# Kernel tuning notes

Hardware: AMD Instinct MI355X
Metric: run time of the kernel (lower is better)

Reference implementation:

```python
import jax, jax.numpy as jnp
import numpy as np

N_EXPERTS = 8
D_IN = 2048
D_OUT = 2048
BATCH = 8192


def setup_inputs() -> dict:
    key = jax.random.key(0)
    k_x, k_w, k_b, k_a, k_m = jax.random.split(key, 5)
    xs = jax.random.normal(k_x, (BATCH, D_IN), dtype=jnp.float32)
    # Expert parameters: each submodule modeled as Linear(D_IN, D_OUT)
    W = jax.random.normal(k_w, (N_EXPERTS, D_IN, D_OUT), dtype=jnp.float32) / np.sqrt(D_IN)
    b = jax.random.normal(k_b, (N_EXPERTS, D_OUT), dtype=jnp.float32) * 0.01
    actions = jax.random.randint(k_a, (BATCH,), 0, N_EXPERTS, dtype=jnp.int32)
    mxs = jax.random.randint(k_m, (BATCH,), 0, N_EXPERTS, dtype=jnp.int32)  # pass-through metadata
    return {"xs": xs, "W": W, "b": b, "mxs": mxs, "actions": actions}


def reference(xs, W, b, mxs, actions):
    # Original: per-sample split, route sample i to submodule actions[i], concat.
    # Vectorized MoE dispatch-combine: compute all expert outputs, select by one-hot.
    onehot = jax.nn.one_hot(actions, W.shape[0], dtype=xs.dtype)  # [B, E]
    # y_all[b,e,f] = xs[b,:] @ W[e,:,:]; combine with one-hot selection, add routed bias.
    ys = jnp.einsum('be,bd,edf->bf', onehot, xs, W) + b[actions]  # [B, D_OUT]
    return (ys, mxs, actions)
```

## Files before the change

### kernel.cpp

```cpp
#include <hip/hip_runtime.h>
#include <hip/hip_bf16.h>
#include <stdint.h>

#define BATCH 8192
#define GROWS 9216
#define DIN   2048
#define DOUT  2048
#define NEXP  8
#define BM    128
#define BN    256
#define BK    32
#define NT    (DIN / BK)
#define NSLOT 72
#define BUFSZ 24576
#define BOFF  8192

typedef __attribute__((ext_vector_type(4))) float fx4;
typedef __attribute__((ext_vector_type(8))) short sx8;

__device__ __forceinline__ short f2b(float x){
  unsigned u = __float_as_uint(x);
  u = u + 0x7FFFu + ((u >> 16) & 1u);
  return (short)(u >> 16);
}

__device__ __forceinline__ void gload16(const void* g, void* l){
  __builtin_amdgcn_global_load_lds(
      (const __attribute__((address_space(1))) unsigned int*)g,
      (__attribute__((address_space(3))) unsigned int*)l, 16, 0, 0);
}

__global__ void prep_kernel(const int* __restrict__ actions, const int* __restrict__ mxs,
                            int* __restrict__ perm, int* __restrict__ meta,
                            float* __restrict__ out){
  __shared__ int cnt[NEXP], cur[NEXP];
  int t = threadIdx.x;
  for (int i = t; i < GROWS; i += 256) perm[i] = -1;
  if (t < NEXP) cnt[t] = 0;
  __syncthreads();
  for (int i = t; i < BATCH; i += 256){
    atomicAdd(&cnt[actions[i]], 1);
    out[(size_t)BATCH * DOUT + i]         = (float)mxs[i];
    out[(size_t)BATCH * DOUT + BATCH + i] = (float)actions[i];
  }
  __syncthreads();
  if (t == 0){
    int s = 0, slot = 0;
    for (int e = 0; e < NEXP; ++e){
      cur[e] = s;
      int ns = (cnt[e] + BM - 1) / BM;
      for (int q = 0; q < ns; ++q) meta[17 + slot++] = e;
      s += ns * BM;
    }
    meta[16] = slot;
  }
  __syncthreads();
  for (int i = t; i < BATCH; i += 256){
    int e = actions[i];
    perm[atomicAdd(&cur[e], 1)] = i;
  }
}

__global__ void gatherx_kernel(const float* __restrict__ xs, const int* __restrict__ perm,
                               short* __restrict__ xp){
  int i = blockIdx.x;
  int t = threadIdx.x;
  short v[8];
  int p = perm[i];
  if (p >= 0){
    const fx4* src = (const fx4*)(xs + (size_t)p * DIN + t * 8);
    fx4 a = src[0], b2 = src[1];
    v[0]=f2b(a.x); v[1]=f2b(a.y); v[2]=f2b(a.z); v[3]=f2b(a.w);
    v[4]=f2b(b2.x); v[5]=f2b(b2.y); v[6]=f2b(b2.z); v[7]=f2b(b2.w);
  } else {
#pragma unroll
    for (int j = 0; j < 8; ++j) v[j] = 0;
  }
  *(sx8*)(xp + (size_t)i * DIN + t * 8) = *(const sx8*)v;
}

__global__ void transw_kernel(const float* __restrict__ W, short* __restrict__ Wt){
  __shared__ float tile[64][69];
  int e  = blockIdx.z;
  int n0 = blockIdx.x * 64;
  int k0 = blockIdx.y * 64;
  const float* Wp = W + (size_t)e * DIN * DOUT + (size_t)k0 * DOUT + n0;
  int t = threadIdx.x;
#pragma unroll
  for (int it = 0; it < 4; ++it){
    int r = it * 16 + (t >> 4);
    int c = (t & 15) * 4;
    fx4 v = *(const fx4*)(Wp + (size_t)r * DOUT + c);
    tile[r][c] = v.x; tile[r][c+1] = v.y; tile[r][c+2] = v.z; tile[r][c+3] = v.w;
  }
  __syncthreads();
  int n  = t >> 2;
  int kc = (t & 3) * 16;
  short vv[16];
#pragma unroll
  for (int j = 0; j < 16; ++j) vv[j] = f2b(tile[kc + j][n]);
  short* dst = Wt + (size_t)e * DOUT * DIN + (size_t)(n0 + n) * DIN + k0 + kc;
  *(sx8*)dst       = *(const sx8*)vv;
  *(sx8*)(dst + 8) = *(const sx8*)(vv + 8);
}

__global__ __launch_bounds__(512, 4)
void moe_gemm_kernel(const short* __restrict__ xp, const short* __restrict__ Wt,
                     const float* __restrict__ bias, const int* __restrict__ perm,
                     const int* __restrict__ meta, float* __restrict__ out){
  __shared__ char lds[3 * BUFSZ];

  int F = blockIdx.x;
  int slot = F >> 3, nb = F & 7;
  int nslots = meta[16];
  if (slot >= nslots) return;
  int e      = meta[17 + slot];
  int m_base = slot * BM;
  int n0     = nb * BN;

  int t    = threadIdx.x;
  int wid  = t >> 6;
  int l    = t & 63;
  int wm   = wid & 1;
  int wn   = wid >> 1;
  int lrow = l & 15;
  int lk   = l >> 4;

  int srow = ((t >> 3) << 1) | ((t >> 2) & 1);
  int schk = (t & 3) ^ ((t >> 3) & 3);
  const char* ag  = (const char*)xp + ((size_t)(m_base + srow) * DIN + schk * 8) * 2;
  const char* bg0 = (const char*)Wt + (((size_t)e * DOUT + n0 + srow) * DIN + schk * 8) * 2;
  const char* bg1 = bg0 + (size_t)128 * DIN * 2;
  int ldst = t * 16;

#define STAGE(kt, BASE) do{ \
    gload16(ag  + (size_t)(kt) * 64, lds + (BASE) + ldst); \
    gload16(bg0 + (size_t)(kt) * 64, lds + (BASE) + BOFF + ldst); \
    gload16(bg1 + (size_t)(kt) * 64, lds + (BASE) + BOFF + 8192 + ldst); \
  }while(0)

  int arow = wm * 64 + lrow;
  int aline = arow >> 1;
  int addrA = aline * 128 + (arow & 1) * 64 + ((lk ^ (aline & 3)) << 4);
  int brow = wn * 64 + lrow;
  int bline = brow >> 1;
  int addrB = BOFF + bline * 128 + (brow & 1) * 64 + ((lk ^ (bline & 3)) << 4);

  fx4 acc[4][4];
#pragma unroll
  for (int m = 0; m < 4; ++m)
#pragma unroll
    for (int n = 0; n < 4; ++n)
      acc[m][n] = (fx4){0.f, 0.f, 0.f, 0.f};

  float bcol[4];
#pragma unroll
  for (int n = 0; n < 4; ++n)
    bcol[n] = bias[(size_t)e * DOUT + n0 + wn * 64 + n * 16 + lrow];

#define KSTEP(CB, SB, DOSTG, kt) do{ \
    sx8 af[4], bf[4]; \
    _Pragma("unroll") for (int m = 0; m < 4; ++m) \
      af[m] = *(const sx8*)(lds + (CB) + addrA + m * 1024); \
    _Pragma("unroll") for (int n = 0; n < 4; ++n) \
      bf[n] = *(const sx8*)(lds + (CB) + addrB + n * 1024); \
    if (DOSTG) STAGE((kt) + 2, SB); \
    __builtin_amdgcn_s_setprio(1); \
    _Pragma("unroll") for (int m = 0; m < 4; ++m) \
    _Pragma("unroll") for (int n = 0; n < 4; ++n) \
      acc[m][n] = __builtin_amdgcn_mfma_f32_16x16x32_bf16(af[m], bf[n], acc[m][n], 0, 0, 0); \
    __builtin_amdgcn_s_setprio(0); \
    if (DOSTG) asm volatile("s_waitcnt vmcnt(3)" ::: "memory"); \
    else       asm volatile("s_waitcnt vmcnt(0)" ::: "memory"); \
    __builtin_amdgcn_s_barrier(); \
    asm volatile("" ::: "memory"); \
  }while(0)

  STAGE(0, 0);
  STAGE(1, BUFSZ);
  asm volatile("s_waitcnt vmcnt(3)" ::: "memory");
  __builtin_amdgcn_s_barrier();
  asm volatile("" ::: "memory");

  for (int kt = 0; kt < 60; kt += 3){
    KSTEP(0,         2*BUFSZ, 1, kt);
    KSTEP(BUFSZ,     0,       1, kt + 1);
    KSTEP(2*BUFSZ,   BUFSZ,   1, kt + 2);
  }
  KSTEP(0,       2*BUFSZ, 1, 60);
  KSTEP(BUFSZ,   0,       1, 61);
  KSTEP(2*BUFSZ, 0,       0, 62);
  KSTEP(0,       0,       0, 63);

#pragma unroll
  for (int m = 0; m < 4; ++m){
    int rb = wm * 64 + m * 16 + lk * 4;
    int prow[4];
#pragma unroll
    for (int q = 0; q < 4; ++q)
      prow[q] = perm[m_base + rb + q];
#pragma unroll
    for (int n = 0; n < 4; ++n){
      int col = n0 + wn * 64 + n * 16 + lrow;
      fx4 v = acc[m][n];
#pragma unroll
      for (int q = 0; q < 4; ++q)
        if (prow[q] >= 0)
          out[(size_t)prow[q] * DOUT + col] = v[q] + bcol[n];
    }
  }
#undef KSTEP
#undef STAGE
}

extern "C" void kernel_launch(void* const* d_in, const int* in_sizes, int n_in,
                              void* d_out, int out_size, void* d_ws, size_t ws_size,
                              hipStream_t stream) {
  const float* xs      = (const float*)d_in[0];
  const float* W       = (const float*)d_in[1];
  const float* b       = (const float*)d_in[2];
  const int*   mxs     = (const int*)d_in[3];
  const int*   actions = (const int*)d_in[4];
  float* out = (float*)d_out;

  int*   perm = (int*)d_ws;
  int*   meta = (int*)((char*)d_ws + 40960);
  short* Wt   = (short*)((char*)d_ws + 65536);
  short* xp   = (short*)((char*)d_ws + 65536 + (size_t)NEXP * DIN * DOUT * 2);

  hipLaunchKernelGGL(prep_kernel, dim3(1), dim3(256), 0, stream, actions, mxs, perm, meta, out);
  hipLaunchKernelGGL(gatherx_kernel, dim3(GROWS), dim3(256), 0, stream, xs, perm, xp);
  hipLaunchKernelGGL(transw_kernel, dim3(DOUT/64, DIN/64, NEXP), dim3(256), 0, stream, W, Wt);
  hipLaunchKernelGGL(moe_gemm_kernel, dim3(NSLOT * 8), dim3(512), 0, stream,
                     xp, Wt, b, perm, meta, out);
}
```

Baseline: 190.5 us.

## Split prep into count and parallel scatter; deepen A prefetch with k-major LDS layout

The single-block prep kernel becomes a 1024-thread count kernel plus a 32-block scatter kernel that uses global atomics on per-expert cursors and also writes the pass-through outputs. The GEMM replaces the swizzled row-major LDS tiles with a k-chunk-major layout, uses separate ring buffers for A (4 deep) and B (3 deep), and prefetches A three tiles ahead. This is meant to cut serial prep time and hide global-load latency better. The costs are an extra kernel launch, a larger LDS footprint (80 KB) that may reduce occupancy, possible LDS bank conflicts from dropping the XOR swizzle, and a nondeterministic row order from the global atomics.

```diff
diff --git a/kernel.cpp b/kernel.cpp
--- a/kernel.cpp
+++ b/kernel.cpp
@@ -12,8 +12,13 @@
 #define BK    32
 #define NT    (DIN / BK)
 #define NSLOT 72
-#define BUFSZ 24576
-#define BOFF  8192
+#define AB0 0
+#define AB1 8192
+#define AB2 16384
+#define AB3 24576
+#define BB0 32768
+#define BB1 49152
+#define BB2 65536
 
 typedef __attribute__((ext_vector_type(4))) float fx4;
 typedef __attribute__((ext_vector_type(8))) short sx8;
@@ -30,34 +35,37 @@
       (__attribute__((address_space(3))) unsigned int*)l, 16, 0, 0);
 }
 
-__global__ void prep_kernel(const int* __restrict__ actions, const int* __restrict__ mxs,
-                            int* __restrict__ perm, int* __restrict__ meta,
-                            float* __restrict__ out){
-  __shared__ int cnt[NEXP], cur[NEXP];
+__global__ void prep_count(const int* __restrict__ actions, int* __restrict__ perm,
+                           int* __restrict__ meta){
+  __shared__ int cnt[NEXP];
   int t = threadIdx.x;
-  for (int i = t; i < GROWS; i += 256) perm[i] = -1;
   if (t < NEXP) cnt[t] = 0;
+  for (int i = t; i < GROWS; i += 1024) perm[i] = -1;
   __syncthreads();
-  for (int i = t; i < BATCH; i += 256){
-    atomicAdd(&cnt[actions[i]], 1);
-    out[(size_t)BATCH * DOUT + i]         = (float)mxs[i];
-    out[(size_t)BATCH * DOUT + BATCH + i] = (float)actions[i];
-  }
+  for (int i = t; i < BATCH; i += 1024) atomicAdd(&cnt[actions[i]], 1);
   __syncthreads();
   if (t == 0){
     int s = 0, slot = 0;
     for (int e = 0; e < NEXP; ++e){
-      cur[e] = s;
+      meta[e] = s;
       int ns = (cnt[e] + BM - 1) / BM;
       for (int q = 0; q < ns; ++q) meta[17 + slot++] = e;
       s += ns * BM;
     }
     meta[16] = slot;
   }
-  __syncthreads();
-  for (int i = t; i < BATCH; i += 256){
+}
+
+__global__ void prep_scatter(const int* __restrict__ actions, const int* __restrict__ mxs,
+                             int* __restrict__ perm, int* __restrict__ meta,
+                             float* __restrict__ out){
+  int i = blockIdx.x * 256 + threadIdx.x;
+  if (i < BATCH){
     int e = actions[i];
-    perm[atomicAdd(&cur[e], 1)] = i;
+    int p = atomicAdd(&meta[e], 1);
+    perm[p] = i;
+    out[(size_t)BATCH * DOUT + i]         = (float)mxs[i];
+    out[(size_t)BATCH * DOUT + BATCH + i] = (float)actions[i];
   }
 }
 
@@ -108,12 +116,11 @@
 void moe_gemm_kernel(const short* __restrict__ xp, const short* __restrict__ Wt,
                      const float* __restrict__ bias, const int* __restrict__ perm,
                      const int* __restrict__ meta, float* __restrict__ out){
-  __shared__ char lds[3 * BUFSZ];
+  __shared__ char lds[81920];
 
   int F = blockIdx.x;
   int slot = F >> 3, nb = F & 7;
-  int nslots = meta[16];
-  if (slot >= nslots) return;
+  if (slot >= meta[16]) return;
   int e      = meta[17 + slot];
   int m_base = slot * BM;
   int n0     = nb * BN;
@@ -126,25 +133,11 @@
   int lrow = l & 15;
   int lk   = l >> 4;
 
-  int srow = ((t >> 3) << 1) | ((t >> 2) & 1);
-  int schk = (t & 3) ^ ((t >> 3) & 3);
-  const char* ag  = (const char*)xp + ((size_t)(m_base + srow) * DIN + schk * 8) * 2;
-  const char* bg0 = (const char*)Wt + (((size_t)e * DOUT + n0 + srow) * DIN + schk * 8) * 2;
-  const char* bg1 = bg0 + (size_t)128 * DIN * 2;
-  int ldst = t * 16;
-
-#define STAGE(kt, BASE) do{ \
-    gload16(ag  + (size_t)(kt) * 64, lds + (BASE) + ldst); \
-    gload16(bg0 + (size_t)(kt) * 64, lds + (BASE) + BOFF + ldst); \
-    gload16(bg1 + (size_t)(kt) * 64, lds + (BASE) + BOFF + 8192 + ldst); \
-  }while(0)
-
-  int arow = wm * 64 + lrow;
-  int aline = arow >> 1;
-  int addrA = aline * 128 + (arow & 1) * 64 + ((lk ^ (aline & 3)) << 4);
-  int brow = wn * 64 + lrow;
-  int bline = brow >> 1;
-  int addrB = BOFF + bline * 128 + (brow & 1) * 64 + ((lk ^ (bline & 3)) << 4);
+  const char* ag = (const char*)xp + ((size_t)(m_base + (t & 127)) * DIN + (t >> 7) * 8) * 2;
+  const char* bg = (const char*)Wt + (((size_t)e * DOUT + n0 + (t & 255)) * DIN + (t >> 8) * 8) * 2;
+
+  int addrA = lk * 2048 + (wm * 64 + lrow) * 16;
+  int addrB = lk * 4096 + (wn * 64 + lrow) * 16;
 
   fx4 acc[4][4];
 #pragma unroll
@@ -158,39 +151,64 @@
   for (int n = 0; n < 4; ++n)
     bcol[n] = bias[(size_t)e * DOUT + n0 + wn * 64 + n * 16 + lrow];
 
-#define KSTEP(CB, SB, DOSTG, kt) do{ \
+#define STGA(KT, SA) gload16(ag + (size_t)(KT) * 64, lds + (SA) + (t << 4))
+#define STGB(KT, SB) do{ gload16(bg + (size_t)(KT) * 64,      lds + (SB) + (t << 4)); \
+                         gload16(bg + (size_t)(KT) * 64 + 32, lds + (SB) + 8192 + (t << 4)); }while(0)
+
+#define KSTEP(CA, CB, SA, SB, KT, DOB, DOA, VM) do{ \
+    if (DOB) STGB((KT) + 2, SB); \
+    if (DOA) STGA((KT) + 3, SA); \
     sx8 af[4], bf[4]; \
     _Pragma("unroll") for (int m = 0; m < 4; ++m) \
-      af[m] = *(const sx8*)(lds + (CB) + addrA + m * 1024); \
+      af[m] = *(const sx8*)(lds + (CA) + addrA + m * 256); \
     _Pragma("unroll") for (int n = 0; n < 4; ++n) \
-      bf[n] = *(const sx8*)(lds + (CB) + addrB + n * 1024); \
-    if (DOSTG) STAGE((kt) + 2, SB); \
+      bf[n] = *(const sx8*)(lds + (CB) + addrB + n * 256); \
     __builtin_amdgcn_s_setprio(1); \
     _Pragma("unroll") for (int m = 0; m < 4; ++m) \
     _Pragma("unroll") for (int n = 0; n < 4; ++n) \
       acc[m][n] = __builtin_amdgcn_mfma_f32_16x16x32_bf16(af[m], bf[n], acc[m][n], 0, 0, 0); \
     __builtin_amdgcn_s_setprio(0); \
-    if (DOSTG) asm volatile("s_waitcnt vmcnt(3)" ::: "memory"); \
-    else       asm volatile("s_waitcnt vmcnt(0)" ::: "memory"); \
+    asm volatile("s_waitcnt vmcnt(" #VM ")" ::: "memory"); \
     __builtin_amdgcn_s_barrier(); \
     asm volatile("" ::: "memory"); \
   }while(0)
 
-  STAGE(0, 0);
-  STAGE(1, BUFSZ);
-  asm volatile("s_waitcnt vmcnt(3)" ::: "memory");
+  STGA(0, AB0); STGB(0, BB0);
+  STGA(1, AB1); STGB(1, BB1);
+  STGA(2, AB2);
+  asm volatile("s_waitcnt vmcnt(4)" ::: "memory");
   __builtin_amdgcn_s_barrier();
   asm volatile("" ::: "memory");
 
-  for (int kt = 0; kt < 60; kt += 3){
-    KSTEP(0,         2*BUFSZ, 1, kt);
-    KSTEP(BUFSZ,     0,       1, kt + 1);
-    KSTEP(2*BUFSZ,   BUFSZ,   1, kt + 2);
-  }
-  KSTEP(0,       2*BUFSZ, 1, 60);
-  KSTEP(BUFSZ,   0,       1, 61);
-  KSTEP(2*BUFSZ, 0,       0, 62);
-  KSTEP(0,       0,       0, 63);
+  for (int kt = 0; kt < 60; kt += 12){
+    KSTEP(AB0, BB0, AB3, BB2, kt + 0,  1, 1, 4);
+    KSTEP(AB1, BB1, AB0, BB0, kt + 1,  1, 1, 4);
+    KSTEP(AB2, BB2, AB1, BB1, kt + 2,  1, 1, 4);
+    KSTEP(AB3, BB0, AB2, BB2, kt + 3,  1, 1, 4);
+    KSTEP(AB0, BB1, AB3, BB0, kt + 4,  1, 1, 4);
+    KSTEP(AB1, BB2, AB0, BB1, kt + 5,  1, 1, 4);
+    KSTEP(AB2, BB0, AB1, BB2, kt + 6,  1, 1, 4);
+    KSTEP(AB3, BB1, AB2, BB0, kt + 7,  1, 1, 4);
+    KSTEP(AB0, BB2, AB3, BB1, kt + 8,  1, 1, 4);
+    KSTEP(AB1, BB0, AB0, BB2, kt + 9,  1, 1, 4);
+    KSTEP(AB2, BB1, AB1, BB0, kt + 10, 1, 1, 4);
+    KSTEP(AB3, BB2, AB2, BB1, kt + 11, 1, 1, 4);
+  }
+  KSTEP(AB0, BB0, AB3, BB2, 60, 1, 1, 4);
+  KSTEP(AB1, BB1, AB0, BB0, 61, 1, 0, 3);
+  KSTEP(AB2, BB2, AB0, BB0, 62, 0, 0, 0);
+  {
+    sx8 af[4], bf[4];
+#pragma unroll
+    for (int m = 0; m < 4; ++m) af[m] = *(const sx8*)(lds + AB3 + addrA + m * 256);
+#pragma unroll
+    for (int n = 0; n < 4; ++n) bf[n] = *(const sx8*)(lds + BB0 + addrB + n * 256);
+#pragma unroll
+    for (int m = 0; m < 4; ++m)
+#pragma unroll
+      for (int n = 0; n < 4; ++n)
+        acc[m][n] = __builtin_amdgcn_mfma_f32_16x16x32_bf16(af[m], bf[n], acc[m][n], 0, 0, 0);
+  }
 
 #pragma unroll
   for (int m = 0; m < 4; ++m){
@@ -210,7 +228,8 @@
     }
   }
 #undef KSTEP
-#undef STAGE
+#undef STGA
+#undef STGB
 }
 
 extern "C" void kernel_launch(void* const* d_in, const int* in_sizes, int n_in,
@@ -228,7 +247,8 @@
   short* Wt   = (short*)((char*)d_ws + 65536);
   short* xp   = (short*)((char*)d_ws + 65536 + (size_t)NEXP * DIN * DOUT * 2);
 
-  hipLaunchKernelGGL(prep_kernel, dim3(1), dim3(256), 0, stream, actions, mxs, perm, meta, out);
+  hipLaunchKernelGGL(prep_count, dim3(1), dim3(1024), 0, stream, actions, perm, meta);
+  hipLaunchKernelGGL(prep_scatter, dim3(32), dim3(256), 0, stream, actions, mxs, perm, meta, out);
   hipLaunchKernelGGL(gatherx_kernel, dim3(GROWS), dim3(256), 0, stream, xs, perm, xp);
   hipLaunchKernelGGL(transw_kernel, dim3(DOUT/64, DIN/64, NEXP), dim3(256), 0, stream, W, Wt);
   hipLaunchKernelGGL(moe_gemm_kernel, dim3(NSLOT * 8), dim3(512), 0, stream,
```

Result: slower. 284.2 us (+49.2%).

## Parallelize routing scatter and make MoE GEMM persistent with atomic tile queue

Applied to the files above, without the earlier changes.

The single-block prep kernel is split in two. A 1024-thread block counts experts and writes slot offsets into meta. A 32-block kernel then scatters the permutation using global atomics and writes the pass-through outputs. The GEMM becomes a persistent kernel of 512 blocks that pull (slot, n-block) work items from an atomic counter, so no blocks are launched only to exit on empty slots. This trades an extra kernel launch and contended global atomics for less serial prep work and dynamic load balancing, though with 512 blocks some blocks process a second tile in a tail round.

```diff
diff --git a/kernel.cpp b/kernel.cpp
--- a/kernel.cpp
+++ b/kernel.cpp
@@ -30,34 +30,38 @@
       (__attribute__((address_space(3))) unsigned int*)l, 16, 0, 0);
 }
 
-__global__ void prep_kernel(const int* __restrict__ actions, const int* __restrict__ mxs,
-                            int* __restrict__ perm, int* __restrict__ meta,
-                            float* __restrict__ out){
-  __shared__ int cnt[NEXP], cur[NEXP];
+__global__ void prep_count(const int* __restrict__ actions, int* __restrict__ perm,
+                           int* __restrict__ meta){
+  __shared__ int cnt[NEXP];
   int t = threadIdx.x;
-  for (int i = t; i < GROWS; i += 256) perm[i] = -1;
   if (t < NEXP) cnt[t] = 0;
+  for (int i = t; i < GROWS; i += 1024) perm[i] = -1;
   __syncthreads();
-  for (int i = t; i < BATCH; i += 256){
-    atomicAdd(&cnt[actions[i]], 1);
-    out[(size_t)BATCH * DOUT + i]         = (float)mxs[i];
-    out[(size_t)BATCH * DOUT + BATCH + i] = (float)actions[i];
-  }
+  for (int i = t; i < BATCH; i += 1024) atomicAdd(&cnt[actions[i]], 1);
   __syncthreads();
   if (t == 0){
     int s = 0, slot = 0;
     for (int e = 0; e < NEXP; ++e){
-      cur[e] = s;
+      meta[e] = s;
       int ns = (cnt[e] + BM - 1) / BM;
       for (int q = 0; q < ns; ++q) meta[17 + slot++] = e;
       s += ns * BM;
     }
     meta[16] = slot;
-  }
-  __syncthreads();
-  for (int i = t; i < BATCH; i += 256){
+    meta[15] = 0;
+  }
+}
+
+__global__ void prep_scatter(const int* __restrict__ actions, const int* __restrict__ mxs,
+                             int* __restrict__ perm, int* __restrict__ meta,
+                             float* __restrict__ out){
+  int i = blockIdx.x * 256 + threadIdx.x;
+  if (i < BATCH){
     int e = actions[i];
-    perm[atomicAdd(&cur[e], 1)] = i;
+    int p = atomicAdd(&meta[e], 1);
+    perm[p] = i;
+    out[(size_t)BATCH * DOUT + i]         = (float)mxs[i];
+    out[(size_t)BATCH * DOUT + BATCH + i] = (float)actions[i];
   }
 }
 
@@ -107,16 +111,11 @@
 __global__ __launch_bounds__(512, 4)
 void moe_gemm_kernel(const short* __restrict__ xp, const short* __restrict__ Wt,
                      const float* __restrict__ bias, const int* __restrict__ perm,
-                     const int* __restrict__ meta, float* __restrict__ out){
+                     int* __restrict__ meta, float* __restrict__ out){
   __shared__ char lds[3 * BUFSZ];
-
-  int F = blockIdx.x;
-  int slot = F >> 3, nb = F & 7;
-  int nslots = meta[16];
-  if (slot >= nslots) return;
-  int e      = meta[17 + slot];
-  int m_base = slot * BM;
-  int n0     = nb * BN;
+  __shared__ int s_item;
+
+  int nitems = meta[16] * 8;
 
   int t    = threadIdx.x;
   int wid  = t >> 6;
@@ -128,16 +127,7 @@
 
   int srow = ((t >> 3) << 1) | ((t >> 2) & 1);
   int schk = (t & 3) ^ ((t >> 3) & 3);
-  const char* ag  = (const char*)xp + ((size_t)(m_base + srow) * DIN + schk * 8) * 2;
-  const char* bg0 = (const char*)Wt + (((size_t)e * DOUT + n0 + srow) * DIN + schk * 8) * 2;
-  const char* bg1 = bg0 + (size_t)128 * DIN * 2;
   int ldst = t * 16;
-
-#define STAGE(kt, BASE) do{ \
-    gload16(ag  + (size_t)(kt) * 64, lds + (BASE) + ldst); \
-    gload16(bg0 + (size_t)(kt) * 64, lds + (BASE) + BOFF + ldst); \
-    gload16(bg1 + (size_t)(kt) * 64, lds + (BASE) + BOFF + 8192 + ldst); \
-  }while(0)
 
   int arow = wm * 64 + lrow;
   int aline = arow >> 1;
@@ -146,17 +136,38 @@
   int bline = brow >> 1;
   int addrB = BOFF + bline * 128 + (brow & 1) * 64 + ((lk ^ (bline & 3)) << 4);
 
-  fx4 acc[4][4];
-#pragma unroll
-  for (int m = 0; m < 4; ++m)
+  for (;;){
+    if (t == 0) s_item = atomicAdd(&meta[15], 1);
+    __syncthreads();
+    int item = s_item;
+    if (item >= nitems) break;
+
+    int slot = item >> 3, nb = item & 7;
+    int e      = meta[17 + slot];
+    int m_base = slot * BM;
+    int n0     = nb * BN;
+
+    const char* ag  = (const char*)xp + ((size_t)(m_base + srow) * DIN + schk * 8) * 2;
+    const char* bg0 = (const char*)Wt + (((size_t)e * DOUT + n0 + srow) * DIN + schk * 8) * 2;
+    const char* bg1 = bg0 + (size_t)128 * DIN * 2;
+
+#define STAGE(kt, BASE) do{ \
+    gload16(ag  + (size_t)(kt) * 64, lds + (BASE) + ldst); \
+    gload16(bg0 + (size_t)(kt) * 64, lds + (BASE) + BOFF + ldst); \
+    gload16(bg1 + (size_t)(kt) * 64, lds + (BASE) + BOFF + 8192 + ldst); \
+  }while(0)
+
+    fx4 acc[4][4];
+#pragma unroll
+    for (int m = 0; m < 4; ++m)
+#pragma unroll
+      for (int n = 0; n < 4; ++n)
+        acc[m][n] = (fx4){0.f, 0.f, 0.f, 0.f};
+
+    float bcol[4];
 #pragma unroll
     for (int n = 0; n < 4; ++n)
-      acc[m][n] = (fx4){0.f, 0.f, 0.f, 0.f};
-
-  float bcol[4];
-#pragma unroll
-  for (int n = 0; n < 4; ++n)
-    bcol[n] = bias[(size_t)e * DOUT + n0 + wn * 64 + n * 16 + lrow];
+      bcol[n] = bias[(size_t)e * DOUT + n0 + wn * 64 + n * 16 + lrow];
 
 #define KSTEP(CB, SB, DOSTG, kt) do{ \
     sx8 af[4], bf[4]; \
@@ -176,41 +187,53 @@
     asm volatile("" ::: "memory"); \
   }while(0)
 
-  STAGE(0, 0);
-  STAGE(1, BUFSZ);
-  asm volatile("s_waitcnt vmcnt(3)" ::: "memory");
-  __builtin_amdgcn_s_barrier();
-  asm volatile("" ::: "memory");
-
-  for (int kt = 0; kt < 60; kt += 3){
-    KSTEP(0,         2*BUFSZ, 1, kt);
-    KSTEP(BUFSZ,     0,       1, kt + 1);
-    KSTEP(2*BUFSZ,   BUFSZ,   1, kt + 2);
-  }
-  KSTEP(0,       2*BUFSZ, 1, 60);
-  KSTEP(BUFSZ,   0,       1, 61);
-  KSTEP(2*BUFSZ, 0,       0, 62);
-  KSTEP(0,       0,       0, 63);
-
-#pragma unroll
-  for (int m = 0; m < 4; ++m){
-    int rb = wm * 64 + m * 16 + lk * 4;
-    int prow[4];
-#pragma unroll
-    for (int q = 0; q < 4; ++q)
-      prow[q] = perm[m_base + rb + q];
-#pragma unroll
-    for (int n = 0; n < 4; ++n){
-      int col = n0 + wn * 64 + n * 16 + lrow;
-      fx4 v = acc[m][n];
+    STAGE(0, 0);
+    STAGE(1, BUFSZ);
+    asm volatile("s_waitcnt vmcnt(3)" ::: "memory");
+    __builtin_amdgcn_s_barrier();
+    asm volatile("" ::: "memory");
+
+    for (int kt = 0; kt < 60; kt += 3){
+      KSTEP(0,         2*BUFSZ, 1, kt);
+      KSTEP(BUFSZ,     0,       1, kt + 1);
+      KSTEP(2*BUFSZ,   BUFSZ,   1, kt + 2);
+    }
+    KSTEP(0,       2*BUFSZ, 1, 60);
+    KSTEP(BUFSZ,   0,       1, 61);
+    KSTEP(2*BUFSZ, 0,       0, 62);
+    {
+      sx8 af[4], bf[4];
+#pragma unroll
+      for (int m = 0; m < 4; ++m) af[m] = *(const sx8*)(lds + addrA + m * 1024);
+#pragma unroll
+      for (int n = 0; n < 4; ++n) bf[n] = *(const sx8*)(lds + addrB + n * 1024);
+#pragma unroll
+      for (int m = 0; m < 4; ++m)
+#pragma unroll
+        for (int n = 0; n < 4; ++n)
+          acc[m][n] = __builtin_amdgcn_mfma_f32_16x16x32_bf16(af[m], bf[n], acc[m][n], 0, 0, 0);
+    }
+
+#pragma unroll
+    for (int m = 0; m < 4; ++m){
+      int rb = wm * 64 + m * 16 + lk * 4;
+      int prow[4];
 #pragma unroll
       for (int q = 0; q < 4; ++q)
-        if (prow[q] >= 0)
-          out[(size_t)prow[q] * DOUT + col] = v[q] + bcol[n];
-    }
-  }
+        prow[q] = perm[m_base + rb + q];
+#pragma unroll
+      for (int n = 0; n < 4; ++n){
+        int col = n0 + wn * 64 + n * 16 + lrow;
+        fx4 v = acc[m][n];
+#pragma unroll
+        for (int q = 0; q < 4; ++q)
+          if (prow[q] >= 0)
+            out[(size_t)prow[q] * DOUT + col] = v[q] + bcol[n];
+      }
+    }
 #undef KSTEP
 #undef STAGE
+  }
 }
 
 extern "C" void kernel_launch(void* const* d_in, const int* in_sizes, int n_in,
@@ -228,9 +251,10 @@
   short* Wt   = (short*)((char*)d_ws + 65536);
   short* xp   = (short*)((char*)d_ws + 65536 + (size_t)NEXP * DIN * DOUT * 2);
 
-  hipLaunchKernelGGL(prep_kernel, dim3(1), dim3(256), 0, stream, actions, mxs, perm, meta, out);
+  hipLaunchKernelGGL(prep_count, dim3(1), dim3(1024), 0, stream, actions, perm, meta);
+  hipLaunchKernelGGL(prep_scatter, dim3(32), dim3(256), 0, stream, actions, mxs, perm, meta, out);
   hipLaunchKernelGGL(gatherx_kernel, dim3(GROWS), dim3(256), 0, stream, xs, perm, xp);
   hipLaunchKernelGGL(transw_kernel, dim3(DOUT/64, DIN/64, NEXP), dim3(256), 0, stream, W, Wt);
-  hipLaunchKernelGGL(moe_gemm_kernel, dim3(NSLOT * 8), dim3(512), 0, stream,
+  hipLaunchKernelGGL(moe_gemm_kernel, dim3(512), dim3(512), 0, stream,
                      xp, Wt, b, perm, meta, out);
 }
```

Result: slower. 209.9 us (+10.1%).
